# Kernel tuning notes

Measured on AMD Instinct MI355X. Metric: run time of the kernel, lower is better.

Reference implementation:

```python
import jax, jax.numpy as jnp
import numpy as np

N, D = 8192, 512
NUM_SOURCES = 8


def setup_inputs() -> dict:
    key = jax.random.key(0)
    k1, k2, k3 = jax.random.split(key, 3)
    image_features = jax.random.normal(k1, (N, D), dtype=jnp.float32)
    text_features = jax.random.normal(k2, (N, D), dtype=jnp.float32)
    logit_scale = jnp.ones((), dtype=jnp.float32)
    source_labels = jax.random.randint(k3, (N,), 0, NUM_SOURCES, dtype=jnp.int64)
    return {
        "image_features": image_features,
        "text_features": text_features,
        "logit_scale": logit_scale,
        "source_labels": source_labels,
    }


def reference(image_features, text_features, logit_scale, source_labels):
    n = source_labels.shape[0]
    # [N, N] logits and row-wise log-softmax
    logits = logit_scale * (image_features @ text_features.T)
    log_probs = jax.nn.log_softmax(logits, axis=1)
    # same-source mask, diagonal excluded
    mask = (source_labels[:, None] == source_labels[None, :]) & (~jnp.eye(n, dtype=bool))
    count_pos = mask.sum(axis=1)  # [N]
    row_sum = jnp.where(mask, log_probs, 0.0).sum(axis=1)  # [N]
    # per-row mean over positives; rows with zero positives contribute 0
    row_mean = jnp.where(count_pos > 0, row_sum / jnp.maximum(count_pos, 1).astype(log_probs.dtype), 0.0)
    # loss = -(sum_i row_mean_i) / N
    return -row_mean.sum() / n
```

## Files before the change

### kernel.cpp

```cpp
#include <hip/hip_runtime.h>
#include <cmath>

#define NN 8192
#define DD 512
#define NSRC 8
#define SPLITS 16
#define BM 128
#define BN 128
#define BK 64
#define CPS (NN / SPLITS)
#define CTILES (CPS / BN)
#define COFF 100.0f

typedef __bf16 bf16x8 __attribute__((ext_vector_type(8)));
typedef float  f32x4  __attribute__((ext_vector_type(4)));

__device__ __forceinline__ unsigned short f2bf(float f) {
    unsigned u = __float_as_uint(f);
    u += 0x7fffu + ((u >> 16) & 1u);
    return (unsigned short)(u >> 16);
}

__global__ __launch_bounds__(256) void k_cast(
    const float* __restrict__ img, const float* __restrict__ txt,
    unsigned short* __restrict__ imgB, unsigned short* __restrict__ txtB,
    float* __restrict__ Tsum, int* __restrict__ counts, float* __restrict__ out)
{
    if (blockIdx.x == 0) {
        float4 z = {0.f, 0.f, 0.f, 0.f};
#pragma unroll
        for (int k = 0; k < 4; k++)
            *(float4*)(Tsum + (k * 256 + threadIdx.x) * 4) = z;
        if (threadIdx.x < NSRC) counts[threadIdx.x] = 0;
        if (threadIdx.x == 0) out[0] = 0.f;
    }
    const size_t gid = (size_t)blockIdx.x * 256 + threadIdx.x;
    const size_t half = (size_t)NN * DD / 8;
    const float* src = (gid < half) ? img : txt;
    unsigned short* dst = (gid < half) ? imgB : txtB;
    const size_t off = ((gid < half) ? gid : gid - half) * 8;
    const float4 v0 = *(const float4*)(src + off);
    const float4 v1 = *(const float4*)(src + off + 4);
    union { unsigned short s[8]; uint4 v; } o;
    o.s[0] = f2bf(v0.x); o.s[1] = f2bf(v0.y); o.s[2] = f2bf(v0.z); o.s[3] = f2bf(v0.w);
    o.s[4] = f2bf(v1.x); o.s[5] = f2bf(v1.y); o.s[6] = f2bf(v1.z); o.s[7] = f2bf(v1.w);
    *(uint4*)(dst + off) = o.v;
}

__global__ __launch_bounds__(256) void k_src_sums(
    const float* __restrict__ txt, const int* __restrict__ labels,
    float* __restrict__ Tsum, int* __restrict__ counts)
{
    __shared__ float Tacc[NSRC * DD];
    __shared__ int cacc[NSRC];
    const int tid = threadIdx.x;
    const int d0 = 2 * tid;
#pragma unroll
    for (int s = 0; s < NSRC; s++) {
        Tacc[s * DD + d0] = 0.f;
        Tacc[s * DD + d0 + 1] = 0.f;
    }
    if (tid < NSRC) cacc[tid] = 0;
    __syncthreads();

    const int row0 = blockIdx.x * 64;
    if (tid < 64) atomicAdd(&cacc[labels[row0 + tid]], 1);

    for (int j = 0; j < 64; j++) {
        const int lab = labels[row0 + j];
        const float2 v = *(const float2*)(txt + (size_t)(row0 + j) * DD + d0);
        Tacc[lab * DD + d0]     += v.x;
        Tacc[lab * DD + d0 + 1] += v.y;
    }
    __syncthreads();
#pragma unroll
    for (int k = 0; k < NSRC * DD / 256; k++) {
        const int e = k * 256 + tid;
        atomicAdd(&Tsum[e], Tacc[e]);
    }
    if (tid < NSRC) atomicAdd(&counts[tid], cacc[tid]);
}

__global__ __launch_bounds__(256) void k_lse_mfma(
    const unsigned short* __restrict__ imgB, const unsigned short* __restrict__ txtB,
    const float* __restrict__ scale_p,
    float* __restrict__ ps)
{
    __shared__ uint4 lds[2048];
    const float scale = scale_p[0];
    const int tid  = threadIdx.x;
    const int lane = tid & 63;
    const int w    = tid >> 6;
    const int split = blockIdx.x & (SPLITS - 1);
    const int by    = blockIdx.x / SPLITS;
    const int row0  = by * BM;
    const int colBase = split * CPS;
    const int lq = lane >> 4;
    const int ln = lane & 15;

    int st_r[4], st_kc[4];
#pragma unroll
    for (int t = 0; t < 4; t++) {
        const int p = t * 256 + tid;
        st_r[t]  = p >> 3;
        st_kc[t] = (p & 7) ^ (st_r[t] & 7);
    }

    int aIdx[2], aSw[2], bIdx[8], bSw[8];
#pragma unroll
    for (int i = 0; i < 2; i++) {
        const int r = w * 32 + i * 16 + ln;
        aIdx[i] = r * 8; aSw[i] = r & 7;
    }
#pragma unroll
    for (int j = 0; j < 8; j++) {
        const int r = j * 16 + ln;
        bIdx[j] = 1024 + r * 8; bSw[j] = r & 7;
    }

    float s_run[2][4];
#pragma unroll
    for (int i = 0; i < 2; i++)
#pragma unroll
        for (int rg = 0; rg < 4; rg++) s_run[i][rg] = 0.f;

    for (int ct = 0; ct < CTILES; ct++) {
        const int col0 = colBase + ct * BN;
        f32x4 acc[2][8];
#pragma unroll
        for (int i = 0; i < 2; i++)
#pragma unroll
            for (int j = 0; j < 8; j++) acc[i][j] = (f32x4){0.f, 0.f, 0.f, 0.f};

        for (int kt = 0; kt < DD; kt += BK) {
            __syncthreads();
#pragma unroll
            for (int t = 0; t < 4; t++) {
                const unsigned short* g =
                    imgB + (size_t)(row0 + st_r[t]) * DD + kt + (st_kc[t] << 3);
                __builtin_amdgcn_global_load_lds(
                    (const __attribute__((address_space(1))) void*)g,
                    (__attribute__((address_space(3))) void*)&lds[t * 256 + (w << 6)],
                    16, 0, 0);
            }
#pragma unroll
            for (int t = 0; t < 4; t++) {
                const unsigned short* g =
                    txtB + (size_t)(col0 + st_r[t]) * DD + kt + (st_kc[t] << 3);
                __builtin_amdgcn_global_load_lds(
                    (const __attribute__((address_space(1))) void*)g,
                    (__attribute__((address_space(3))) void*)&lds[1024 + t * 256 + (w << 6)],
                    16, 0, 0);
            }
            __syncthreads();
#pragma unroll
            for (int ks = 0; ks < 2; ks++) {
                bf16x8 af[2], bf[8];
#pragma unroll
                for (int i = 0; i < 2; i++)
                    af[i] = *reinterpret_cast<const bf16x8*>(
                        &lds[aIdx[i] + (((ks << 2) + lq) ^ aSw[i])]);
#pragma unroll
                for (int j = 0; j < 8; j++)
                    bf[j] = *reinterpret_cast<const bf16x8*>(
                        &lds[bIdx[j] + (((ks << 2) + lq) ^ bSw[j])]);
#pragma unroll
                for (int i = 0; i < 2; i++)
#pragma unroll
                    for (int j = 0; j < 8; j++)
                        acc[i][j] = __builtin_amdgcn_mfma_f32_16x16x32_bf16(
                            af[i], bf[j], acc[i][j], 0, 0, 0);
            }
        }
#pragma unroll
        for (int i = 0; i < 2; i++)
#pragma unroll
        for (int rg = 0; rg < 4; rg++) {
            float es = s_run[i][rg];
#pragma unroll
            for (int j = 0; j < 8; j++)
                es += __expf(fmaf(acc[i][j][rg], scale, -COFF));
            s_run[i][rg] = es;
        }
    }
#pragma unroll
    for (int i = 0; i < 2; i++)
#pragma unroll
    for (int rg = 0; rg < 4; rg++) {
        float es = s_run[i][rg];
#pragma unroll
        for (int off = 8; off; off >>= 1) es += __shfl_xor(es, off);
        s_run[i][rg] = es;
    }
    if (ln == 0) {
#pragma unroll
        for (int i = 0; i < 2; i++)
#pragma unroll
        for (int rg = 0; rg < 4; rg++) {
            const int row = row0 + w * 32 + i * 16 + lq * 4 + rg;
            ps[(size_t)row * SPLITS + split] = s_run[i][rg];
        }
    }
}

__global__ __launch_bounds__(256) void k_finalize(
    const float* __restrict__ img, const float* __restrict__ txt,
    const int* __restrict__ labels, const float* __restrict__ scale_p,
    const float* __restrict__ Tsum, const int* __restrict__ counts,
    const float* __restrict__ ps,
    float* __restrict__ out)
{
    const float scale = scale_p[0];
    const int tid = threadIdx.x;
    const int lane = tid & 63;
    const int wave = tid >> 6;
    const int rowBase = blockIdx.x * 16 + wave * 4;
    float local = 0.f;
#pragma unroll
    for (int it = 0; it < 4; it++) {
        const int i = rowBase + it;
        const int lab = labels[i];
        float ds = 0.f, dt = 0.f;
        const float* ip = img + (size_t)i * DD;
        const float* tp = txt + (size_t)i * DD;
        const float* sp = Tsum + lab * DD;
#pragma unroll
        for (int k = lane; k < DD; k += 64) {
            const float a = ip[k];
            ds = fmaf(a, tp[k], ds);
            dt = fmaf(a, sp[k], dt);
        }
#pragma unroll
        for (int off = 32; off; off >>= 1) {
            ds += __shfl_xor(ds, off);
            dt += __shfl_xor(dt, off);
        }
        if (lane == 0) {
            float ssum = 0.f;
#pragma unroll
            for (int s = 0; s < SPLITS; s++)
                ssum += ps[(size_t)i * SPLITS + s];
            const float lse = COFF + __logf(ssum);
            const int cnt = counts[lab] - 1;
            if (cnt > 0) {
                const float row_sum = scale * (dt - ds) - (float)cnt * lse;
                local += row_sum / (float)cnt;
            }
        }
    }
    __shared__ float red[4];
    if (lane == 0) red[wave] = local;
    __syncthreads();
    if (tid == 0) {
        const float t = red[0] + red[1] + red[2] + red[3];
        atomicAdd(out, -t / (float)NN);
    }
}

extern "C" void kernel_launch(void* const* d_in, const int* in_sizes, int n_in,
                              void* d_out, int out_size, void* d_ws, size_t ws_size,
                              hipStream_t stream)
{
    const float* img     = (const float*)d_in[0];
    const float* txt     = (const float*)d_in[1];
    const float* scale_p = (const float*)d_in[2];
    const int*   labels  = (const int*)d_in[3];
    float* out = (float*)d_out;

    char* ws = (char*)d_ws;
    float* ps    = (float*)(ws);
    float* Tsum  = (float*)(ws + (size_t)NN * SPLITS * 4);
    int*   counts = (int*)(ws + (size_t)NN * SPLITS * 4 + NSRC * DD * 4);
    unsigned short* imgB = (unsigned short*)(ws + 2 * 1024 * 1024);
    unsigned short* txtB = (unsigned short*)(ws + 10 * 1024 * 1024);

    k_cast<<<(2 * NN * DD / 8) / 256, 256, 0, stream>>>(img, txt, imgB, txtB,
                                                        Tsum, counts, out);
    k_src_sums<<<NN / 64, 256, 0, stream>>>(txt, labels, Tsum, counts);
    k_lse_mfma<<<(NN / BM) * SPLITS, 256, 0, stream>>>(imgB, txtB, scale_p, ps);
    k_finalize<<<NN / 16, 256, 0, stream>>>(img, txt, labels, scale_p,
                                            Tsum, counts, ps, out);
}
```

Baseline: 188.0 us.

## Switch logits GEMM to 32x32x16 MFMA, atomic row sums, register source sums

```diff
diff --git a/kernel.cpp b/kernel.cpp
--- a/kernel.cpp
+++ b/kernel.cpp
@@ -13,7 +13,7 @@
 #define COFF 100.0f
 
 typedef __bf16 bf16x8 __attribute__((ext_vector_type(8)));
-typedef float  f32x4  __attribute__((ext_vector_type(4)));
+typedef float  f32x16 __attribute__((ext_vector_type(16)));
 
 __device__ __forceinline__ unsigned short f2bf(float f) {
     unsigned u = __float_as_uint(f);
@@ -24,10 +24,14 @@
 __global__ __launch_bounds__(256) void k_cast(
     const float* __restrict__ img, const float* __restrict__ txt,
     unsigned short* __restrict__ imgB, unsigned short* __restrict__ txtB,
-    float* __restrict__ Tsum, int* __restrict__ counts, float* __restrict__ out)
+    float* __restrict__ ps, float* __restrict__ Tsum,
+    int* __restrict__ counts, float* __restrict__ out)
 {
     if (blockIdx.x == 0) {
-        float4 z = {0.f, 0.f, 0.f, 0.f};
+        const float4 z = {0.f, 0.f, 0.f, 0.f};
+#pragma unroll
+        for (int k = 0; k < 8; k++)
+            *(float4*)(ps + (k * 256 + threadIdx.x) * 4) = z;
 #pragma unroll
         for (int k = 0; k < 4; k++)
             *(float4*)(Tsum + (k * 256 + threadIdx.x) * 4) = z;
@@ -51,37 +55,38 @@
     const float* __restrict__ txt, const int* __restrict__ labels,
     float* __restrict__ Tsum, int* __restrict__ counts)
 {
-    __shared__ float Tacc[NSRC * DD];
-    __shared__ int cacc[NSRC];
     const int tid = threadIdx.x;
     const int d0 = 2 * tid;
-#pragma unroll
-    for (int s = 0; s < NSRC; s++) {
-        Tacc[s * DD + d0] = 0.f;
-        Tacc[s * DD + d0 + 1] = 0.f;
-    }
+    const int row0 = blockIdx.x * 64;
+    float accx[NSRC], accy[NSRC];
+#pragma unroll
+    for (int s = 0; s < NSRC; s++) { accx[s] = 0.f; accy[s] = 0.f; }
+
+    __shared__ int cacc[NSRC];
     if (tid < NSRC) cacc[tid] = 0;
     __syncthreads();
-
-    const int row0 = blockIdx.x * 64;
     if (tid < 64) atomicAdd(&cacc[labels[row0 + tid]], 1);
 
+#pragma unroll 4
     for (int j = 0; j < 64; j++) {
         const int lab = labels[row0 + j];
         const float2 v = *(const float2*)(txt + (size_t)(row0 + j) * DD + d0);
-        Tacc[lab * DD + d0]     += v.x;
-        Tacc[lab * DD + d0 + 1] += v.y;
+#pragma unroll
+        for (int s = 0; s < NSRC; s++) {
+            accx[s] += (lab == s) ? v.x : 0.f;
+            accy[s] += (lab == s) ? v.y : 0.f;
+        }
+    }
+#pragma unroll
+    for (int s = 0; s < NSRC; s++) {
+        atomicAdd(&Tsum[s * DD + d0],     accx[s]);
+        atomicAdd(&Tsum[s * DD + d0 + 1], accy[s]);
     }
     __syncthreads();
-#pragma unroll
-    for (int k = 0; k < NSRC * DD / 256; k++) {
-        const int e = k * 256 + tid;
-        atomicAdd(&Tsum[e], Tacc[e]);
-    }
     if (tid < NSRC) atomicAdd(&counts[tid], cacc[tid]);
 }
 
-__global__ __launch_bounds__(256) void k_lse_mfma(
+__global__ __launch_bounds__(256, 4) void k_lse_mfma(
     const unsigned short* __restrict__ imgB, const unsigned short* __restrict__ txtB,
     const float* __restrict__ scale_p,
     float* __restrict__ ps)
@@ -95,8 +100,8 @@
     const int by    = blockIdx.x / SPLITS;
     const int row0  = by * BM;
     const int colBase = split * CPS;
-    const int lq = lane >> 4;
-    const int ln = lane & 15;
+    const int lo = lane & 31;
+    const int hi = lane >> 5;
 
     int st_r[4], st_kc[4];
 #pragma unroll
@@ -106,31 +111,26 @@
         st_kc[t] = (p & 7) ^ (st_r[t] & 7);
     }
 
-    int aIdx[2], aSw[2], bIdx[8], bSw[8];
-#pragma unroll
-    for (int i = 0; i < 2; i++) {
-        const int r = w * 32 + i * 16 + ln;
-        aIdx[i] = r * 8; aSw[i] = r & 7;
-    }
-#pragma unroll
-    for (int j = 0; j < 8; j++) {
-        const int r = j * 16 + ln;
-        bIdx[j] = 1024 + r * 8; bSw[j] = r & 7;
-    }
-
-    float s_run[2][4];
-#pragma unroll
-    for (int i = 0; i < 2; i++)
-#pragma unroll
-        for (int rg = 0; rg < 4; rg++) s_run[i][rg] = 0.f;
+    const int ar = w * 32 + lo;
+    const int aIdx = ar * 8, aSw = ar & 7;
+    int bIdx[4], bSw[4];
+#pragma unroll
+    for (int j = 0; j < 4; j++) {
+        const int c = j * 32 + lo;
+        bIdx[j] = 1024 + c * 8; bSw[j] = c & 7;
+    }
+
+    float s_run[16];
+#pragma unroll
+    for (int rg = 0; rg < 16; rg++) s_run[rg] = 0.f;
 
     for (int ct = 0; ct < CTILES; ct++) {
         const int col0 = colBase + ct * BN;
-        f32x4 acc[2][8];
-#pragma unroll
-        for (int i = 0; i < 2; i++)
-#pragma unroll
-            for (int j = 0; j < 8; j++) acc[i][j] = (f32x4){0.f, 0.f, 0.f, 0.f};
+        f32x16 acc[4];
+#pragma unroll
+        for (int j = 0; j < 4; j++)
+#pragma unroll
+            for (int rg = 0; rg < 16; rg++) acc[j][rg] = 0.f;
 
         for (int kt = 0; kt < DD; kt += BK) {
             __syncthreads();
@@ -154,51 +154,39 @@
             }
             __syncthreads();
 #pragma unroll
-            for (int ks = 0; ks < 2; ks++) {
-                bf16x8 af[2], bf[8];
-#pragma unroll
-                for (int i = 0; i < 2; i++)
-                    af[i] = *reinterpret_cast<const bf16x8*>(
-                        &lds[aIdx[i] + (((ks << 2) + lq) ^ aSw[i])]);
-#pragma unroll
-                for (int j = 0; j < 8; j++)
+            for (int ks = 0; ks < 4; ks++) {
+                const int kc = ks * 2 + hi;
+                const bf16x8 af = *reinterpret_cast<const bf16x8*>(
+                    &lds[aIdx + (kc ^ aSw)]);
+                bf16x8 bf[4];
+#pragma unroll
+                for (int j = 0; j < 4; j++)
                     bf[j] = *reinterpret_cast<const bf16x8*>(
-                        &lds[bIdx[j] + (((ks << 2) + lq) ^ bSw[j])]);
-#pragma unroll
-                for (int i = 0; i < 2; i++)
-#pragma unroll
-                    for (int j = 0; j < 8; j++)
-                        acc[i][j] = __builtin_amdgcn_mfma_f32_16x16x32_bf16(
-                            af[i], bf[j], acc[i][j], 0, 0, 0);
-            }
-        }
-#pragma unroll
-        for (int i = 0; i < 2; i++)
-#pragma unroll
-        for (int rg = 0; rg < 4; rg++) {
-            float es = s_run[i][rg];
-#pragma unroll
-            for (int j = 0; j < 8; j++)
-                es += __expf(fmaf(acc[i][j][rg], scale, -COFF));
-            s_run[i][rg] = es;
-        }
-    }
-#pragma unroll
-    for (int i = 0; i < 2; i++)
-#pragma unroll
-    for (int rg = 0; rg < 4; rg++) {
-        float es = s_run[i][rg];
-#pragma unroll
-        for (int off = 8; off; off >>= 1) es += __shfl_xor(es, off);
-        s_run[i][rg] = es;
-    }
-    if (ln == 0) {
-#pragma unroll
-        for (int i = 0; i < 2; i++)
-#pragma unroll
-        for (int rg = 0; rg < 4; rg++) {
-            const int row = row0 + w * 32 + i * 16 + lq * 4 + rg;
-            ps[(size_t)row * SPLITS + split] = s_run[i][rg];
+                        &lds[bIdx[j] + (kc ^ bSw[j])]);
+#pragma unroll
+                for (int j = 0; j < 4; j++)
+                    acc[j] = __builtin_amdgcn_mfma_f32_32x32x16_bf16(
+                        af, bf[j], acc[j], 0, 0, 0);
+            }
+        }
+#pragma unroll
+        for (int j = 0; j < 4; j++)
+#pragma unroll
+        for (int rg = 0; rg < 16; rg++)
+            s_run[rg] += __expf(fmaf(acc[j][rg], scale, -COFF));
+    }
+#pragma unroll
+    for (int rg = 0; rg < 16; rg++) {
+        float es = s_run[rg];
+#pragma unroll
+        for (int off = 16; off; off >>= 1) es += __shfl_xor(es, off);
+        s_run[rg] = es;
+    }
+    if (lo == 0) {
+#pragma unroll
+        for (int rg = 0; rg < 16; rg++) {
+            const int row = row0 + w * 32 + (rg & 3) + 8 * (rg >> 2) + 4 * hi;
+            atomicAdd(&ps[row], s_run[rg]);
         }
     }
 }
@@ -236,11 +224,7 @@
             dt += __shfl_xor(dt, off);
         }
         if (lane == 0) {
-            float ssum = 0.f;
-#pragma unroll
-            for (int s = 0; s < SPLITS; s++)
-                ssum += ps[(size_t)i * SPLITS + s];
-            const float lse = COFF + __logf(ssum);
+            const float lse = COFF + __logf(ps[i]);
             const int cnt = counts[lab] - 1;
             if (cnt > 0) {
                 const float row_sum = scale * (dt - ds) - (float)cnt * lse;
@@ -269,13 +253,13 @@
 
     char* ws = (char*)d_ws;
     float* ps    = (float*)(ws);
-    float* Tsum  = (float*)(ws + (size_t)NN * SPLITS * 4);
-    int*   counts = (int*)(ws + (size_t)NN * SPLITS * 4 + NSRC * DD * 4);
+    float* Tsum  = (float*)(ws + (size_t)NN * 4);
+    int*   counts = (int*)(ws + (size_t)NN * 4 + NSRC * DD * 4);
     unsigned short* imgB = (unsigned short*)(ws + 2 * 1024 * 1024);
     unsigned short* txtB = (unsigned short*)(ws + 10 * 1024 * 1024);
 
     k_cast<<<(2 * NN * DD / 8) / 256, 256, 0, stream>>>(img, txt, imgB, txtB,
-                                                        Tsum, counts, out);
+                                                        ps, Tsum, counts, out);
     k_src_sums<<<NN / 64, 256, 0, stream>>>(txt, labels, Tsum, counts);
     k_lse_mfma<<<(NN / BM) * SPLITS, 256, 0, stream>>>(imgB, txtB, scale_p, ps);
     k_finalize<<<NN / 16, 256, 0, stream>>>(img, txt, labels, scale_p,
```

Measured after the change: 196.3 us. +4.4%, slower.
